# Optimization experiments

Hardware: AMD Instinct MI355X
Metric: run time of the kernel (lower is better)

## Reference

```python
import jax, jax.numpy as jnp
import numpy as np

NUM_HEADS = 16
HEAD_SIZE = 128


def _alibi_mask(seq_len: int, num_heads: int) -> jnp.ndarray:
    # slopes: num_heads > 8 branch -> 1 / 2**(i/2)
    if num_heads <= 8:
        slopes = jnp.asarray([1.0 / 2.0 ** i for i in range(num_heads)], dtype=jnp.float32)
    else:
        slopes = jnp.asarray([1.0 / 2.0 ** (i / 2.0) for i in range(num_heads)], dtype=jnp.float32)
    i = jnp.arange(seq_len)[:, None]
    j = jnp.arange(seq_len)[None, :]
    # -(i-j) on/below diagonal, -inf strictly above (causal)
    base = jnp.where(j <= i, -(i - j).astype(jnp.float32), -jnp.inf)  # [S, S]
    return slopes[:, None, None] * base  # [H, S, S]; slope * -inf = -inf


def setup_inputs() -> dict:
    key = jax.random.key(0)
    ks = jax.random.split(key, 5)
    H = 2048
    s = 0.02
    return {
        "x": jax.random.normal(ks[0], (2, 2048, H), dtype=jnp.float32),
        "qkv_w": jax.random.normal(ks[1], (H, 3 * NUM_HEADS * HEAD_SIZE), dtype=jnp.float32) * s,
        "qkv_b": jax.random.normal(ks[2], (3 * NUM_HEADS * HEAD_SIZE,), dtype=jnp.float32) * s,
        "out_w": jax.random.normal(ks[3], (NUM_HEADS * HEAD_SIZE, H), dtype=jnp.float32) * s,
        "out_b": jax.random.normal(ks[4], (H,), dtype=jnp.float32) * s,
    }


def reference(x, qkv_w, qkv_b, out_w, out_b):
    b, s, h = x.shape
    qkv = x @ qkv_w + qkv_b  # [b, s, 3*H*D]
    q, k, v = jnp.split(qkv, 3, axis=-1)

    def to_heads(t):
        return t.reshape(b, s, NUM_HEADS, HEAD_SIZE).transpose(0, 2, 1, 3)  # [b,h,s,d]

    q, k, v = to_heads(q), to_heads(k), to_heads(v)
    # NOTE: original module does NOT scale by 1/sqrt(d)
    scores = jnp.einsum("bhid,bhjd->bhij", q, k) + _alibi_mask(s, NUM_HEADS)[None]
    attn = jax.nn.softmax(scores, axis=-1)
    ctx = jnp.einsum("bhij,bhjd->bhid", attn, v)  # [b,h,s,d]
    ctx = ctx.transpose(0, 2, 1, 3).reshape(b, s, NUM_HEADS * HEAD_SIZE)
    return ctx @ out_w + out_b
```

## Files before the change

kernel.cpp:

```cpp
#include <hip/hip_runtime.h>

typedef _Float16 h8 __attribute__((ext_vector_type(8)));
typedef _Float16 h4 __attribute__((ext_vector_type(4)));
typedef float f4 __attribute__((ext_vector_type(4)));

#define MFMA16(a, b, c) __builtin_amdgcn_mfma_f32_16x16x32_f16((a), (b), (c), 0, 0, 0)
#define AS1 __attribute__((address_space(1)))
#define AS3 __attribute__((address_space(3)))

static __device__ __forceinline__ void load_lds16(const _Float16* g, _Float16* l) {
  __builtin_amdgcn_global_load_lds((const AS1 void*)g, (AS3 void*)l, 16, 0, 0);
}

__global__ __launch_bounds__(256) void cvt_f32_f16(const float* __restrict__ in,
                                                   _Float16* __restrict__ out, int n) {
  int i = (blockIdx.x * 256 + threadIdx.x) * 4;
  if (i < n) {
    const float4 v = *(const float4*)(in + i);
    h4 o;
    o[0] = (_Float16)v.x; o[1] = (_Float16)v.y; o[2] = (_Float16)v.z; o[3] = (_Float16)v.w;
    *(h4*)(out + i) = o;
  }
}

__global__ __launch_bounds__(256) void transpose_cvt(const float* __restrict__ W,
                                                     _Float16* __restrict__ Wt, int K, int N) {
  __shared__ _Float16 t[64][66];
  int n0 = blockIdx.x * 64, k0 = blockIdx.y * 64;
  int c = threadIdx.x & 63, r0 = threadIdx.x >> 6;
  for (int i = 0; i < 16; i++) {
    int r = r0 * 16 + i;
    t[r][c] = (_Float16)W[(size_t)(k0 + r) * N + n0 + c];
  }
  __syncthreads();
  for (int i = 0; i < 16; i++) {
    int r = r0 * 16 + i;
    Wt[(size_t)(n0 + r) * K + k0 + c] = t[c][r];
  }
}

template <int MODE>
__global__ __launch_bounds__(256, 2) void gemm_bt(const _Float16* __restrict__ A,
                                               const _Float16* __restrict__ Bt,
                                               const float* __restrict__ bias, int K,
                                               _Float16* __restrict__ qp, _Float16* __restrict__ kp,
                                               _Float16* __restrict__ vtp, float* __restrict__ outp,
                                               int N) {
  __shared__ _Float16 LDS[2][16384];
  const int m0 = blockIdx.y * 128, n0 = blockIdx.x * 128;
  const int tid = threadIdx.x;
  const int w = tid >> 6, lane = tid & 63, quad = lane >> 4, l16 = lane & 15;
  const int wm = (w >> 1) * 64, wn = (w & 1) * 64;

  const int lc8 = (((lane & 7) ^ (lane >> 3)) * 8);
  const int rb = w * 32 + (lane >> 3);
  const _Float16* ap0 = A + (size_t)(m0 + rb) * K + lc8;
  const _Float16* bp0 = Bt + (size_t)(n0 + rb) * K + lc8;

  f4 acc[4][4] = {};
#pragma unroll
  for (int i = 0; i < 4; i++) {
    load_lds16(ap0 + (size_t)(i * 8) * K, &LDS[0][w * 2048 + i * 512]);
    load_lds16(bp0 + (size_t)(i * 8) * K, &LDS[0][8192 + w * 2048 + i * 512]);
  }
  for (int k0 = 0; k0 < K; k0 += 64) {
    const int cur = (k0 >> 6) & 1;
    __syncthreads();
    if (k0 + 64 < K) {
      const int nb = cur ^ 1;
#pragma unroll
      for (int i = 0; i < 4; i++) {
        load_lds16(ap0 + (size_t)(i * 8) * K + k0 + 64, &LDS[nb][w * 2048 + i * 512]);
        load_lds16(bp0 + (size_t)(i * 8) * K + k0 + 64, &LDS[nb][8192 + w * 2048 + i * 512]);
      }
    }
    const _Float16* As = &LDS[cur][0];
    const _Float16* Bs = &LDS[cur][8192];
#pragma unroll
    for (int ks = 0; ks < 2; ks++) {
      h8 af[4], bf[4];
      for (int mi = 0; mi < 4; mi++) {
        int r = wm + mi * 16 + l16;
        int pc = (ks * 4 + quad) ^ (l16 & 7);
        af[mi] = *(const h8*)(&As[r * 64 + pc * 8]);
      }
      for (int ni = 0; ni < 4; ni++) {
        int r = wn + ni * 16 + l16;
        int pc = (ks * 4 + quad) ^ (l16 & 7);
        bf[ni] = *(const h8*)(&Bs[r * 64 + pc * 8]);
      }
      for (int mi = 0; mi < 4; mi++)
        for (int ni = 0; ni < 4; ni++) acc[mi][ni] = MFMA16(af[mi], bf[ni], acc[mi][ni]);
    }
  }

  if constexpr (MODE == 0) {
    __syncthreads();
    _Float16* U = &LDS[0][0];
    const int which = n0 >> 11, hh = (n0 >> 7) & 15;
    const int bq = m0 >> 11, ms = m0 & 2047;
    const size_t hb = (size_t)bq * 16 + hh;
    if (which == 2) {
      for (int mi = 0; mi < 4; mi++)
        for (int ni = 0; ni < 4; ni++) {
          int d = wn + ni * 16 + l16;
          int s0 = wm + mi * 16 + quad * 4;
          float bv = bias[n0 + d];
          h4 pack;
          for (int r = 0; r < 4; r++) pack[r] = (_Float16)(acc[mi][ni][r] + bv);
          *(h4*)(&U[d * 136 + s0]) = pack;
        }
    } else {
      for (int mi = 0; mi < 4; mi++)
        for (int ni = 0; ni < 4; ni++) {
          int d = wn + ni * 16 + l16;
          float bv = bias[n0 + d];
          for (int r = 0; r < 4; r++) {
            int s = wm + mi * 16 + quad * 4 + r;
            U[s * 136 + d] = (_Float16)(acc[mi][ni][r] + bv);
          }
        }
    }
    __syncthreads();
    if (which == 2) {
      _Float16* dst = vtp + hb * (size_t)(128 * 2048) + ms;
#pragma unroll
      for (int i = 0; i < 8; i++) {
        int f = i * 256 + tid, row = f >> 4, ch = f & 15;
        *(h8*)(dst + (size_t)row * 2048 + ch * 8) = *(h8*)(&U[row * 136 + ch * 8]);
      }
    } else {
      _Float16* dst = (which == 0 ? qp : kp) + (hb * 2048 + ms) * (size_t)128;
#pragma unroll
      for (int i = 0; i < 8; i++) {
        int f = i * 256 + tid, row = f >> 4, ch = f & 15;
        *(h8*)(dst + (size_t)row * 128 + ch * 8) = *(h8*)(&U[row * 136 + ch * 8]);
      }
    }
  } else {
    for (int mi = 0; mi < 4; mi++)
      for (int ni = 0; ni < 4; ni++) {
        int gm_base = m0 + wm + mi * 16 + quad * 4;
        int gn = n0 + wn + ni * 16 + l16;
        float bv = bias[gn];
        for (int r = 0; r < 4; r++)
          outp[(size_t)(gm_base + r) * N + gn] = acc[mi][ni][r] + bv;
      }
  }
}

__global__ __launch_bounds__(256, 2) void attn_kernel(const _Float16* __restrict__ Q,
                                                      const _Float16* __restrict__ Kg,
                                                      const _Float16* __restrict__ Vt,
                                                      _Float16* __restrict__ ctx) {
  __shared__ _Float16 Ks[2][8192];
  __shared__ _Float16 Vs[2][8192];
  __shared__ _Float16 Vones[1088];
  __shared__ _Float16 Pl[4][16 * 68];

  const int bh = blockIdx.x, px = blockIdx.y;
  const int b = bh >> 4, h = bh & 15;
  const int tid = threadIdx.x, w = tid >> 6, lane = tid & 63, quad = lane >> 4, l16 = lane & 15;
  const size_t hbo = (size_t)bh * (2048 * 128);
  const _Float16* Qh = Q + hbo;
  const _Float16* Kh = Kg + hbo;
  const _Float16* Vh = Vt + hbo;
  const float slope = exp2f(-0.5f * (float)h);
  const float L2E = 1.44269504088896f;
  const float NEG = -3.0e38f;

  for (int i = tid; i < 1088; i += 256) Vones[i] = (_Float16)0.f;
  if (tid < 64) Vones[tid] = (_Float16)1.f;

  float cj[4];
  for (int jf = 0; jf < 4; jf++) cj[jf] = slope * (float)(jf * 16 + l16);

  const int kle = (l16 ^ quad) * 8, klo = kle ^ 32;
  const int lq = lane >> 3, vlc = ((lane & 7) ^ lq) * 8;

  for (int phase = 0; phase < 2; phase++) {
    const int t = phase ? px : 31 - px;
    const int qbase = t * 64 + w * 16;

    h8 aq[4];
#pragma unroll
    for (int t4 = 0; t4 < 4; t4++)
      aq[t4] = *(const h8*)(Qh + (size_t)(qbase + l16) * 128 + t4 * 32 + quad * 8);

    f4 o[9] = {};
    float m_i[4];
    for (int r = 0; r < 4; r++) m_i[r] = NEG;

    const int jtiles = t + 1;
    __syncthreads();
    if (w < 2) {
      const _Float16* kb = Kh + (size_t)(32 * w + quad) * 128;
      _Float16* dst = &Ks[0][w * 4096];
#pragma unroll
      for (int cc = 0; cc < 8; cc++)
        load_lds16(kb + (size_t)(4 * cc) * 128 + ((cc & 1) ? klo : kle), dst + cc * 512);
    } else {
      const _Float16* vb = Vh + (size_t)(64 * (w - 2) + lq) * 2048 + vlc;
      _Float16* dst = &Vs[0][(w - 2) * 4096];
#pragma unroll
      for (int cc = 0; cc < 8; cc++) load_lds16(vb + (size_t)(8 * cc) * 2048, dst + cc * 512);
    }

    for (int jt = 0; jt < jtiles; jt++) {
      const int j0 = jt * 64, cur = jt & 1;
      __syncthreads();
      if (jt + 1 < jtiles) {
        const int nj0 = j0 + 64, nb = cur ^ 1;
        if (w < 2) {
          const _Float16* kb = Kh + (size_t)(nj0 + 32 * w + quad) * 128;
          _Float16* dst = &Ks[nb][w * 4096];
#pragma unroll
          for (int cc = 0; cc < 8; cc++)
            load_lds16(kb + (size_t)(4 * cc) * 128 + ((cc & 1) ? klo : kle), dst + cc * 512);
        } else {
          const _Float16* vb = Vh + (size_t)(64 * (w - 2) + lq) * 2048 + nj0 + vlc;
          _Float16* dst = &Vs[nb][(w - 2) * 4096];
#pragma unroll
          for (int cc = 0; cc < 8; cc++) load_lds16(vb + (size_t)(8 * cc) * 2048, dst + cc * 512);
        }
      }
      f4 sc[4] = {};
#pragma unroll
      for (int jf = 0; jf < 4; jf++) {
        const int row = jf * 16 + l16;
#pragma unroll
        for (int t4 = 0; t4 < 4; t4++) {
          const int p = (t4 * 4 + quad) ^ (l16 & 7);
          h8 bk = *(const h8*)(&Ks[cur][row * 128 + p * 8]);
          sc[jf] = MFMA16(aq[t4], bk, sc[jf]);
        }
      }
      const float bj0 = slope * (float)j0;
#pragma unroll
      for (int jf = 0; jf < 4; jf++) {
        const float cb = bj0 + cj[jf];
#pragma unroll
        for (int r = 0; r < 4; r++) sc[jf][r] += cb;
      }
      if (jt == jtiles - 1) {
#pragma unroll
        for (int jf = 0; jf < 4; jf++) {
          const int j = j0 + jf * 16 + l16;
#pragma unroll
          for (int r = 0; r < 4; r++)
            if (j > qbase + quad * 4 + r) sc[jf][r] = NEG;
        }
      }
      float m_new[4], alpha[4];
#pragma unroll
      for (int r = 0; r < 4; r++) {
        float v = fmaxf(fmaxf(sc[0][r], sc[1][r]), fmaxf(sc[2][r], sc[3][r]));
        v = fmaxf(v, __shfl_xor(v, 1));
        v = fmaxf(v, __shfl_xor(v, 2));
        v = fmaxf(v, __shfl_xor(v, 4));
        v = fmaxf(v, __shfl_xor(v, 8));
        m_new[r] = fmaxf(m_i[r], v);
        alpha[r] = exp2f((m_i[r] - m_new[r]) * L2E);
        m_i[r] = m_new[r];
      }
#pragma unroll
      for (int jf = 0; jf < 4; jf++)
#pragma unroll
        for (int r = 0; r < 4; r++) sc[jf][r] = exp2f((sc[jf][r] - m_new[r]) * L2E);
#pragma unroll
      for (int nt = 0; nt < 9; nt++)
#pragma unroll
        for (int r = 0; r < 4; r++) o[nt][r] *= alpha[r];
#pragma unroll
      for (int jf = 0; jf < 4; jf++)
#pragma unroll
        for (int r = 0; r < 4; r++)
          Pl[w][(quad * 4 + r) * 68 + jf * 16 + l16] = (_Float16)sc[jf][r];
      asm volatile("s_waitcnt lgkmcnt(0)" ::: "memory");
      h8 ap0 = *(const h8*)(&Pl[w][l16 * 68 + quad * 8]);
      h8 ap1 = *(const h8*)(&Pl[w][l16 * 68 + 32 + quad * 8]);
#pragma unroll
      for (int nt = 0; nt < 8; nt++) {
        const int row = nt * 16 + l16;
        const int p0 = quad ^ (l16 & 7), p1 = (4 + quad) ^ (l16 & 7);
        h8 bv0 = *(const h8*)(&Vs[cur][row * 64 + p0 * 8]);
        h8 bv1 = *(const h8*)(&Vs[cur][row * 64 + p1 * 8]);
        o[nt] = MFMA16(ap0, bv0, o[nt]);
        o[nt] = MFMA16(ap1, bv1, o[nt]);
      }
      {
        h8 b0 = *(const h8*)(&Vones[l16 * 68 + quad * 8]);
        h8 b1 = *(const h8*)(&Vones[l16 * 68 + 32 + quad * 8]);
        o[8] = MFMA16(ap0, b0, o[8]);
        o[8] = MFMA16(ap1, b1, o[8]);
      }
    }

#pragma unroll
    for (int r = 0; r < 4; r++) {
      float lsum = __shfl(o[8][r], lane & 48);
      float inv = 1.0f / lsum;
      const int i = qbase + quad * 4 + r;
      const size_t row = (size_t)b * 2048 + i;
#pragma unroll
      for (int nt = 0; nt < 8; nt++)
        ctx[row * 2048 + h * 128 + nt * 16 + l16] = (_Float16)(o[nt][r] * inv);
    }
  }
}

extern "C" void kernel_launch(void* const* d_in, const int* in_sizes, int n_in, void* d_out,
                              int out_size, void* d_ws, size_t ws_size, hipStream_t stream) {
  const float* x = (const float*)d_in[0];
  const float* qkv_w = (const float*)d_in[1];
  const float* qkv_b = (const float*)d_in[2];
  const float* out_w = (const float*)d_in[3];
  const float* out_b = (const float*)d_in[4];
  float* out = (float*)d_out;

  char* ws = (char*)d_ws;
  if (ws_size < 117440512u) return;
  _Float16* xb  = (_Float16*)(ws + 0);
  _Float16* wqt = (_Float16*)(ws + 16777216);
  _Float16* wot = (_Float16*)(ws + 41943040);
  _Float16* q   = (_Float16*)(ws + 50331648);
  _Float16* k   = (_Float16*)(ws + 67108864);
  _Float16* vt  = (_Float16*)(ws + 83886080);
  _Float16* ctx = (_Float16*)(ws + 100663296);

  cvt_f32_f16<<<8192, 256, 0, stream>>>(x, xb, 8388608);
  transpose_cvt<<<dim3(96, 32), 256, 0, stream>>>(qkv_w, wqt, 2048, 6144);
  transpose_cvt<<<dim3(32, 32), 256, 0, stream>>>(out_w, wot, 2048, 2048);
  gemm_bt<0><<<dim3(48, 32), 256, 0, stream>>>(xb, wqt, qkv_b, 2048, q, k, vt, nullptr, 6144);
  attn_kernel<<<dim3(32, 16), 256, 0, stream>>>(q, k, vt, ctx);
  gemm_bt<1><<<dim3(16, 32), 256, 0, stream>>>(ctx, wot, out_b, 2048, nullptr, nullptr, nullptr,
                                               out, 2048);
}
```

Measured before the change: 379.1 us.

## Enlarge GEMM tiles to 128x256 with 512 threads and triple-buffered LDS pipeline

The projection GEMMs now use 128x256 output tiles computed by 8 waves, cutting redundant A-tile loads and halving the block count. The LDS staging goes from double to triple buffering, with explicit vmcnt waits and raw barriers so two stages of global-to-LDS loads stay in flight. MFMA sections also get raised wave priority. The QKV epilogue writes the wider tile in two 128-column passes through shared memory, which adds extra barriers. It also needs more LDS per block, which may lower occupancy.

New measurement: 393.5 us. +3.8%, slower.

```diff
diff --git a/kernel.cpp b/kernel.cpp
--- a/kernel.cpp
+++ b/kernel.cpp
@@ -40,111 +40,152 @@
 }
 
 template <int MODE>
-__global__ __launch_bounds__(256, 2) void gemm_bt(const _Float16* __restrict__ A,
-                                               const _Float16* __restrict__ Bt,
-                                               const float* __restrict__ bias, int K,
-                                               _Float16* __restrict__ qp, _Float16* __restrict__ kp,
-                                               _Float16* __restrict__ vtp, float* __restrict__ outp,
-                                               int N) {
-  __shared__ _Float16 LDS[2][16384];
-  const int m0 = blockIdx.y * 128, n0 = blockIdx.x * 128;
+__global__ __launch_bounds__(512, 2) void gemm_bt(const _Float16* __restrict__ A,
+                                                  const _Float16* __restrict__ Bt,
+                                                  const float* __restrict__ bias, int K,
+                                                  _Float16* __restrict__ qp,
+                                                  _Float16* __restrict__ kp,
+                                                  _Float16* __restrict__ vtp,
+                                                  float* __restrict__ outp, int N) {
+  __shared__ __align__(16) _Float16 LDS[3][24576];
+  const int m0 = blockIdx.y * 128, n0 = blockIdx.x * 256;
   const int tid = threadIdx.x;
   const int w = tid >> 6, lane = tid & 63, quad = lane >> 4, l16 = lane & 15;
-  const int wm = (w >> 1) * 64, wn = (w & 1) * 64;
-
-  const int lc8 = (((lane & 7) ^ (lane >> 3)) * 8);
-  const int rb = w * 32 + (lane >> 3);
-  const _Float16* ap0 = A + (size_t)(m0 + rb) * K + lc8;
-  const _Float16* bp0 = Bt + (size_t)(n0 + rb) * K + lc8;
+  const int wmo = (w >> 2) * 64, wno = (w & 3) * 64;
+  const int qq = lane >> 3, bb = lane & 7;
+  const int lc8 = (bb ^ qq) * 8;
+
+  const _Float16* ap0 = A + (size_t)(m0 + w * 16 + qq) * K + lc8;
+  const _Float16* bp0 = Bt + (size_t)(n0 + w * 32 + qq) * K + lc8;
+  const int wA = w * 1024, wB = 8192 + w * 2048;
 
   f4 acc[4][4] = {};
-#pragma unroll
-  for (int i = 0; i < 4; i++) {
-    load_lds16(ap0 + (size_t)(i * 8) * K, &LDS[0][w * 2048 + i * 512]);
-    load_lds16(bp0 + (size_t)(i * 8) * K, &LDS[0][8192 + w * 2048 + i * 512]);
-  }
-  for (int k0 = 0; k0 < K; k0 += 64) {
-    const int cur = (k0 >> 6) & 1;
-    __syncthreads();
-    if (k0 + 64 < K) {
-      const int nb = cur ^ 1;
-#pragma unroll
-      for (int i = 0; i < 4; i++) {
-        load_lds16(ap0 + (size_t)(i * 8) * K + k0 + 64, &LDS[nb][w * 2048 + i * 512]);
-        load_lds16(bp0 + (size_t)(i * 8) * K + k0 + 64, &LDS[nb][8192 + w * 2048 + i * 512]);
-      }
-    }
-    const _Float16* As = &LDS[cur][0];
-    const _Float16* Bs = &LDS[cur][8192];
+  const int nk = K >> 6;
+
+#define STAGE(slot, koff)                               \
+  {                                                     \
+    const _Float16* ap = ap0 + (koff);                  \
+    const _Float16* bp = bp0 + (koff);                  \
+    _Float16* la = &LDS[slot][wA];                      \
+    _Float16* lb = &LDS[slot][wB];                      \
+    load_lds16(ap, la);                                 \
+    load_lds16(ap + (size_t)8 * K, la + 512);           \
+    load_lds16(bp, lb);                                 \
+    load_lds16(bp + (size_t)8 * K, lb + 512);           \
+    load_lds16(bp + (size_t)16 * K, lb + 1024);         \
+    load_lds16(bp + (size_t)24 * K, lb + 1536);         \
+  }
+
+  STAGE(0, 0);
+  STAGE(1, 64);
+  asm volatile("s_waitcnt vmcnt(6)" ::: "memory");
+  __builtin_amdgcn_s_barrier();
+
+  int cb = 0, sb = 2;
+  for (int t = 0; t < nk; ++t) {
+    if (t + 2 < nk) STAGE(sb, (t + 2) * 64);
+    sb = cb;
+    const _Float16* As = &LDS[cb][0];
+    const _Float16* Bs = &LDS[cb][8192];
 #pragma unroll
     for (int ks = 0; ks < 2; ks++) {
       h8 af[4], bf[4];
+#pragma unroll
       for (int mi = 0; mi < 4; mi++) {
-        int r = wm + mi * 16 + l16;
-        int pc = (ks * 4 + quad) ^ (l16 & 7);
+        const int r = wmo + mi * 16 + l16;
+        const int pc = (ks * 4 + quad) ^ (l16 & 7);
         af[mi] = *(const h8*)(&As[r * 64 + pc * 8]);
       }
+#pragma unroll
       for (int ni = 0; ni < 4; ni++) {
-        int r = wn + ni * 16 + l16;
-        int pc = (ks * 4 + quad) ^ (l16 & 7);
+        const int r = wno + ni * 16 + l16;
+        const int pc = (ks * 4 + quad) ^ (l16 & 7);
         bf[ni] = *(const h8*)(&Bs[r * 64 + pc * 8]);
       }
+      __builtin_amdgcn_s_setprio(1);
+#pragma unroll
       for (int mi = 0; mi < 4; mi++)
+#pragma unroll
         for (int ni = 0; ni < 4; ni++) acc[mi][ni] = MFMA16(af[mi], bf[ni], acc[mi][ni]);
-    }
-  }
+      __builtin_amdgcn_s_setprio(0);
+    }
+    if (t + 1 < nk) {
+      if (t + 2 < nk)
+        asm volatile("s_waitcnt vmcnt(6)" ::: "memory");
+      else
+        asm volatile("s_waitcnt vmcnt(0)" ::: "memory");
+      __builtin_amdgcn_s_barrier();
+    }
+    cb = (cb == 2) ? 0 : cb + 1;
+  }
+#undef STAGE
 
   if constexpr (MODE == 0) {
-    __syncthreads();
     _Float16* U = &LDS[0][0];
-    const int which = n0 >> 11, hh = (n0 >> 7) & 15;
+    const int which = n0 >> 11;
     const int bq = m0 >> 11, ms = m0 & 2047;
-    const size_t hb = (size_t)bq * 16 + hh;
-    if (which == 2) {
-      for (int mi = 0; mi < 4; mi++)
-        for (int ni = 0; ni < 4; ni++) {
-          int d = wn + ni * 16 + l16;
-          int s0 = wm + mi * 16 + quad * 4;
-          float bv = bias[n0 + d];
-          h4 pack;
-          for (int r = 0; r < 4; r++) pack[r] = (_Float16)(acc[mi][ni][r] + bv);
-          *(h4*)(&U[d * 136 + s0]) = pack;
-        }
-    } else {
-      for (int mi = 0; mi < 4; mi++)
-        for (int ni = 0; ni < 4; ni++) {
-          int d = wn + ni * 16 + l16;
-          float bv = bias[n0 + d];
-          for (int r = 0; r < 4; r++) {
-            int s = wm + mi * 16 + quad * 4 + r;
-            U[s * 136 + d] = (_Float16)(acc[mi][ni][r] + bv);
-          }
-        }
-    }
-    __syncthreads();
-    if (which == 2) {
-      _Float16* dst = vtp + hb * (size_t)(128 * 2048) + ms;
-#pragma unroll
-      for (int i = 0; i < 8; i++) {
-        int f = i * 256 + tid, row = f >> 4, ch = f & 15;
-        *(h8*)(dst + (size_t)row * 2048 + ch * 8) = *(h8*)(&U[row * 136 + ch * 8]);
-      }
-    } else {
-      _Float16* dst = (which == 0 ? qp : kp) + (hb * 2048 + ms) * (size_t)128;
-#pragma unroll
-      for (int i = 0; i < 8; i++) {
-        int f = i * 256 + tid, row = f >> 4, ch = f & 15;
-        *(h8*)(dst + (size_t)row * 128 + ch * 8) = *(h8*)(&U[row * 136 + ch * 8]);
+    const int wn_ = w & 3;
+    const int grp = wn_ >> 1, cl = (wn_ & 1) * 64;
+    for (int g = 0; g < 2; ++g) {
+      __syncthreads();
+      if (grp == g) {
+        if (which == 2) {
+#pragma unroll
+          for (int mi = 0; mi < 4; mi++)
+#pragma unroll
+            for (int ni = 0; ni < 4; ni++) {
+              const int d = cl + ni * 16 + l16;
+              const float bv = bias[n0 + g * 128 + d];
+              const int s0 = wmo + mi * 16 + quad * 4;
+              h4 pack;
+#pragma unroll
+              for (int r = 0; r < 4; r++) pack[r] = (_Float16)(acc[mi][ni][r] + bv);
+              *(h4*)(&U[d * 136 + s0]) = pack;
+            }
+        } else {
+#pragma unroll
+          for (int mi = 0; mi < 4; mi++)
+#pragma unroll
+            for (int ni = 0; ni < 4; ni++) {
+              const int d = cl + ni * 16 + l16;
+              const float bv = bias[n0 + g * 128 + d];
+#pragma unroll
+              for (int r = 0; r < 4; r++) {
+                const int s = wmo + mi * 16 + quad * 4 + r;
+                U[s * 136 + d] = (_Float16)(acc[mi][ni][r] + bv);
+              }
+            }
+        }
+      }
+      __syncthreads();
+      const int hh = ((n0 + g * 128) >> 7) & 15;
+      const size_t hb = (size_t)bq * 16 + hh;
+      if (which == 2) {
+        _Float16* dst = vtp + hb * (size_t)(128 * 2048) + ms;
+#pragma unroll
+        for (int i = 0; i < 4; i++) {
+          int f = i * 512 + tid, row = f >> 4, ch = f & 15;
+          *(h8*)(dst + (size_t)row * 2048 + ch * 8) = *(h8*)(&U[row * 136 + ch * 8]);
+        }
+      } else {
+        _Float16* dst = (which == 0 ? qp : kp) + (hb * 2048 + ms) * (size_t)128;
+#pragma unroll
+        for (int i = 0; i < 4; i++) {
+          int f = i * 512 + tid, row = f >> 4, ch = f & 15;
+          *(h8*)(dst + (size_t)row * 128 + ch * 8) = *(h8*)(&U[row * 136 + ch * 8]);
+        }
       }
     }
   } else {
+#pragma unroll
     for (int mi = 0; mi < 4; mi++)
+#pragma unroll
       for (int ni = 0; ni < 4; ni++) {
-        int gm_base = m0 + wm + mi * 16 + quad * 4;
-        int gn = n0 + wn + ni * 16 + l16;
-        float bv = bias[gn];
-        for (int r = 0; r < 4; r++)
-          outp[(size_t)(gm_base + r) * N + gn] = acc[mi][ni][r] + bv;
+        const int gm = m0 + wmo + mi * 16 + quad * 4;
+        const int gn = n0 + wno + ni * 16 + l16;
+        const float bv = bias[gn];
+#pragma unroll
+        for (int r = 0; r < 4; r++) outp[(size_t)(gm + r) * N + gn] = acc[mi][ni][r] + bv;
       }
   }
 }
@@ -331,8 +372,8 @@
   cvt_f32_f16<<<8192, 256, 0, stream>>>(x, xb, 8388608);
   transpose_cvt<<<dim3(96, 32), 256, 0, stream>>>(qkv_w, wqt, 2048, 6144);
   transpose_cvt<<<dim3(32, 32), 256, 0, stream>>>(out_w, wot, 2048, 2048);
-  gemm_bt<0><<<dim3(48, 32), 256, 0, stream>>>(xb, wqt, qkv_b, 2048, q, k, vt, nullptr, 6144);
+  gemm_bt<0><<<dim3(24, 32), 512, 0, stream>>>(xb, wqt, qkv_b, 2048, q, k, vt, nullptr, 6144);
   attn_kernel<<<dim3(32, 16), 256, 0, stream>>>(q, k, vt, ctx);
-  gemm_bt<1><<<dim3(16, 32), 256, 0, stream>>>(ctx, wot, out_b, 2048, nullptr, nullptr, nullptr,
-                                               out, 2048);
-}
+  gemm_bt<1><<<dim3(8, 32), 512, 0, stream>>>(ctx, wot, out_b, 2048, nullptr, nullptr, nullptr,
+                                              out, 2048);
+}
```

## Halve GEMM K-tile to 32 and raise occupancy to four blocks per CU

Applied to the files above, without the earlier changes.

The projection GEMM now stages K-slices of 32 instead of 64, which cuts shared memory per block from 64KB to about 34KB so launch bounds can request 4 blocks per CU instead of 2. The LDS swizzle and load mapping are reworked for 32-wide rows, and s_setprio brackets the MFMA burst. The aim is more resident waves to hide load latency, at the cost of twice as many barriers per K and less MFMA work between syncs.

Result: slower. 392.8 us (+3.6%).

```diff
diff --git a/kernel.cpp b/kernel.cpp
--- a/kernel.cpp
+++ b/kernel.cpp
@@ -40,63 +40,67 @@
 }
 
 template <int MODE>
-__global__ __launch_bounds__(256, 2) void gemm_bt(const _Float16* __restrict__ A,
-                                               const _Float16* __restrict__ Bt,
-                                               const float* __restrict__ bias, int K,
-                                               _Float16* __restrict__ qp, _Float16* __restrict__ kp,
-                                               _Float16* __restrict__ vtp, float* __restrict__ outp,
-                                               int N) {
-  __shared__ _Float16 LDS[2][16384];
+__global__ __launch_bounds__(256, 4) void gemm_bt(const _Float16* __restrict__ A,
+                                                  const _Float16* __restrict__ Bt,
+                                                  const float* __restrict__ bias, int K,
+                                                  _Float16* __restrict__ qp,
+                                                  _Float16* __restrict__ kp,
+                                                  _Float16* __restrict__ vtp,
+                                                  float* __restrict__ outp, int N) {
+  __shared__ __align__(16) _Float16 SH[17408];
   const int m0 = blockIdx.y * 128, n0 = blockIdx.x * 128;
   const int tid = threadIdx.x;
   const int w = tid >> 6, lane = tid & 63, quad = lane >> 4, l16 = lane & 15;
   const int wm = (w >> 1) * 64, wn = (w & 1) * 64;
 
-  const int lc8 = (((lane & 7) ^ (lane >> 3)) * 8);
-  const int rb = w * 32 + (lane >> 3);
-  const _Float16* ap0 = A + (size_t)(m0 + rb) * K + lc8;
-  const _Float16* bp0 = Bt + (size_t)(n0 + rb) * K + lc8;
+  const int srow = tid >> 2;
+  const int scol = ((tid & 3) ^ ((tid >> 2) & 3)) * 8;
+  const _Float16* Ag = A + (size_t)(m0 + srow) * K + scol;
+  const _Float16* Bg = Bt + (size_t)(n0 + srow) * K + scol;
 
   f4 acc[4][4] = {};
-#pragma unroll
-  for (int i = 0; i < 4; i++) {
-    load_lds16(ap0 + (size_t)(i * 8) * K, &LDS[0][w * 2048 + i * 512]);
-    load_lds16(bp0 + (size_t)(i * 8) * K, &LDS[0][8192 + w * 2048 + i * 512]);
-  }
-  for (int k0 = 0; k0 < K; k0 += 64) {
-    const int cur = (k0 >> 6) & 1;
+  const int NT = K >> 5;
+
+#define STG(b, T)                                                              \
+  {                                                                            \
+    const size_t ko = (size_t)(T) * 32;                                        \
+    load_lds16(Ag + ko, SH + (b) * 8192 + w * 512);                            \
+    load_lds16(Ag + ko + (size_t)64 * K, SH + (b) * 8192 + 2048 + w * 512);    \
+    load_lds16(Bg + ko, SH + (b) * 8192 + 4096 + w * 512);                     \
+    load_lds16(Bg + ko + (size_t)64 * K, SH + (b) * 8192 + 6144 + w * 512);    \
+  }
+
+  STG(0, 0);
+  for (int T = 0; T < NT; ++T) {
+    const int cur = T & 1;
     __syncthreads();
-    if (k0 + 64 < K) {
-      const int nb = cur ^ 1;
-#pragma unroll
-      for (int i = 0; i < 4; i++) {
-        load_lds16(ap0 + (size_t)(i * 8) * K + k0 + 64, &LDS[nb][w * 2048 + i * 512]);
-        load_lds16(bp0 + (size_t)(i * 8) * K + k0 + 64, &LDS[nb][8192 + w * 2048 + i * 512]);
-      }
-    }
-    const _Float16* As = &LDS[cur][0];
-    const _Float16* Bs = &LDS[cur][8192];
-#pragma unroll
-    for (int ks = 0; ks < 2; ks++) {
-      h8 af[4], bf[4];
-      for (int mi = 0; mi < 4; mi++) {
-        int r = wm + mi * 16 + l16;
-        int pc = (ks * 4 + quad) ^ (l16 & 7);
-        af[mi] = *(const h8*)(&As[r * 64 + pc * 8]);
-      }
-      for (int ni = 0; ni < 4; ni++) {
-        int r = wn + ni * 16 + l16;
-        int pc = (ks * 4 + quad) ^ (l16 & 7);
-        bf[ni] = *(const h8*)(&Bs[r * 64 + pc * 8]);
-      }
-      for (int mi = 0; mi < 4; mi++)
-        for (int ni = 0; ni < 4; ni++) acc[mi][ni] = MFMA16(af[mi], bf[ni], acc[mi][ni]);
-    }
-  }
+    if (T + 1 < NT) STG(cur ^ 1, T + 1);
+    const _Float16* As = SH + cur * 8192;
+    const _Float16* Bs = As + 4096;
+    h8 af[4], bf[4];
+    const int pc8 = (quad ^ (l16 & 3)) * 8;
+#pragma unroll
+    for (int mi = 0; mi < 4; mi++) {
+      const int r = wm + mi * 16 + l16;
+      af[mi] = *(const h8*)(&As[r * 32 + pc8]);
+    }
+#pragma unroll
+    for (int ni = 0; ni < 4; ni++) {
+      const int r = wn + ni * 16 + l16;
+      bf[ni] = *(const h8*)(&Bs[r * 32 + pc8]);
+    }
+    __builtin_amdgcn_s_setprio(1);
+#pragma unroll
+    for (int mi = 0; mi < 4; mi++)
+#pragma unroll
+      for (int ni = 0; ni < 4; ni++) acc[mi][ni] = MFMA16(af[mi], bf[ni], acc[mi][ni]);
+    __builtin_amdgcn_s_setprio(0);
+  }
+#undef STG
 
   if constexpr (MODE == 0) {
     __syncthreads();
-    _Float16* U = &LDS[0][0];
+    _Float16* U = SH;
     const int which = n0 >> 11, hh = (n0 >> 7) & 15;
     const int bq = m0 >> 11, ms = m0 & 2047;
     const size_t hb = (size_t)bq * 16 + hh;
```
